# Optimization experiments

Measured on AMD Instinct MI355X. Metric: run time of the kernel, lower is better.

Reference implementation:

```python
import jax, jax.numpy as jnp
import numpy as np

N_NODES = 50000
N_EDGES = 600000
CH = 128


def _mlp(h, w1, b1, w2, b2):
    # Linear -> ReLU -> Linear (weights stored [in, out])
    return jax.nn.relu(h @ w1 + b1) @ w2 + b2


def setup_inputs() -> dict:
    key = jax.random.key(0)
    ks = jax.random.split(key, 12)
    def lin(k, fan_in, fan_out):
        bound = 1.0 / np.sqrt(fan_in)
        kw, kb = jax.random.split(k)
        w = jax.random.uniform(kw, (fan_in, fan_out), jnp.float32, -bound, bound)
        b = jax.random.uniform(kb, (fan_out,), jnp.float32, -bound, bound)
        return w, b
    ew1, eb1 = lin(ks[0], 3 * CH, CH)
    ew2, eb2 = lin(ks[1], CH, CH)
    nw1, nb1 = lin(ks[2], 2 * CH, CH)
    nw2, nb2 = lin(ks[3], CH, CH)
    x = jax.random.normal(ks[4], (N_NODES, CH), jnp.float32)
    edge_attr = jax.random.normal(ks[5], (N_EDGES, CH), jnp.float32)
    edge_index = jax.random.randint(ks[6], (2, N_EDGES), 0, N_NODES, jnp.int64 if jax.config.read('jax_enable_x64') else jnp.int32)
    return {"x": x, "edge_index": edge_index, "edge_attr": edge_attr,
            "ew1": ew1, "eb1": eb1, "ew2": ew2, "eb2": eb2,
            "nw1": nw1, "nb1": nb1, "nw2": nw2, "nb2": nb2}


def reference(x, edge_index, edge_attr, ew1, eb1, ew2, eb2, nw1, nb1, nw2, nb2):
    row, col = edge_index[0], edge_index[1]
    n = x.shape[0]
    # edge model: concat(source, target, edge_attr) -> MLP -> new edge_attr
    e_in = jnp.concatenate([x[row], x[col], edge_attr], axis=1)  # [E, 3*ch]
    new_edge_attr = _mlp(e_in, ew1, eb1, ew2, eb2)               # [E, ch]
    # node model: concat(x[col], new_edge_attr) -> MLP -> scatter_mean over row
    n_in = jnp.concatenate([x[col], new_edge_attr], axis=1)      # [E, 2*ch]
    msg = _mlp(n_in, nw1, nb1, nw2, nb2)                         # [E, ch]
    seg_sum = jax.ops.segment_sum(msg, row, num_segments=n)      # [N, ch]
    cnt = jax.ops.segment_sum(jnp.ones((msg.shape[0],), msg.dtype), row, num_segments=n)
    new_x = seg_sum / jnp.maximum(cnt, 1.0)[:, None]             # scatter_mean
    return new_x, new_edge_attr
```

## Files before the change

### kernel.cpp

```cpp
#include <hip/hip_runtime.h>
#include <stdint.h>

#define NN 50000
#define NE 600000
#define CH 128
#define RT 2
#define EPB 128

typedef __attribute__((ext_vector_type(8))) short short8;
typedef __attribute__((ext_vector_type(4))) float f32x4;
typedef __attribute__((ext_vector_type(4))) uint32_t u32x4;

__device__ __forceinline__ ushort f2bf(float f) {
  union { float f; uint32_t u; } v; v.f = f;
  uint32_t u = v.u;
  return (ushort)((u + 0x7FFFu + ((u >> 16) & 1u)) >> 16);
}
__device__ __forceinline__ float bf2f(uint32_t u16) {
  union { uint32_t u; float f; } t; t.u = u16 << 16; return t.f;
}
__device__ __forceinline__ uint32_t cvtpk_bf16(float a, float b) {
  uint32_t r;
  asm("v_cvt_pk_bf16_f32 %0, %1, %2" : "=v"(r) : "v"(a), "v"(b));
  return r;
}

__global__ void prep_frag_k(const float* __restrict__ ew1, const float* __restrict__ ew2,
                            const float* __restrict__ nw1, const float* __restrict__ nw2,
                            ushort* __restrict__ wB) {
  int idx = blockIdx.x * 256 + threadIdx.x;
  if (idx >= 114688) return;
  const float* src; int local;
  if (idx < 49152)      { src = ew1; local = idx; }
  else if (idx < 65536) { src = ew2; local = idx - 49152; }
  else if (idx < 98304) { src = nw1; local = idx - 65536; }
  else                  { src = nw2; local = idx - 98304; }
  int ks   = local >> 12;
  int rem  = local & 4095;
  int nt   = rem >> 9;
  int t    = rem & 511;
  int lane = t >> 3, i = t & 7;
  int k = ks * 32 + (lane >> 4) * 8 + i;
  int n = nt * 16 + (lane & 15);
  wB[idx] = f2bf(src[k * 128 + n]);
}

__global__ void convert_x_k(const float* __restrict__ x, ushort* __restrict__ xb) {
  int i = blockIdx.x * 256 + threadIdx.x;
  if (i >= NN * CH / 4) return;
  const float4 f = reinterpret_cast<const float4*>(x)[i];
  ushort4 r;
  r.x = f2bf(f.x); r.y = f2bf(f.y); r.z = f2bf(f.z); r.w = f2bf(f.w);
  reinterpret_cast<ushort4*>(xb)[i] = r;
}

__global__ void rank_k(const int* __restrict__ ei, unsigned* __restrict__ cnt,
                       unsigned* __restrict__ rank) {
  int e = blockIdx.x * 256 + threadIdx.x;
  if (e < NE) rank[e] = atomicAdd(&cnt[ei[e]], 1u);
}

__global__ void scan_k(const unsigned* __restrict__ cnt, unsigned* __restrict__ start) {
  __shared__ unsigned s[1024];
  const int CHUNK = (NN + 1023) / 1024;
  int t = threadIdx.x;
  int lo = t * CHUNK, hi = lo + CHUNK < NN ? lo + CHUNK : NN;
  unsigned sum = 0;
  for (int i = lo; i < hi; ++i) sum += cnt[i];
  s[t] = sum;
  __syncthreads();
  for (int off = 1; off < 1024; off <<= 1) {
    unsigned v = (t >= off) ? s[t - off] : 0u;
    __syncthreads();
    s[t] += v;
    __syncthreads();
  }
  unsigned run = t ? s[t - 1] : 0u;
  for (int i = lo; i < hi; ++i) { start[i] = run; run += cnt[i]; }
}

__global__ void dest_k(const int* __restrict__ ei, const unsigned* __restrict__ start,
                       const unsigned* __restrict__ rank, unsigned* __restrict__ dest) {
  int e = blockIdx.x * 256 + threadIdx.x;
  if (e < NE) dest[e] = start[ei[e]] + rank[e];
}

__device__ __forceinline__ void mm8(const ushort* Bcbuf, int lane,
                                    const short8 a[RT], f32x4 acc[RT][8]) {
#pragma unroll
  for (int nt = 0; nt < 8; ++nt) {
    short8 b = *reinterpret_cast<const short8*>(Bcbuf + nt * 512 + lane * 8);
#pragma unroll
    for (int rt = 0; rt < RT; ++rt)
      acc[rt][nt] = __builtin_amdgcn_mfma_f32_16x16x32_bf16(a[rt], b, acc[rt][nt], 0, 0, 0);
  }
}

__global__ __launch_bounds__(256, 2) void fused_k(
    const int* __restrict__ ei, const float* __restrict__ edge_attr,
    const ushort* __restrict__ wB,
    const float* __restrict__ eb1, const float* __restrict__ eb2,
    const float* __restrict__ nb1, const float* __restrict__ nb2,
    const ushort* __restrict__ xb, const unsigned* __restrict__ dest,
    ushort* __restrict__ msg, float* __restrict__ out_e)
{
  __shared__ ushort hbuf[4][RT * 16][136];
  __shared__ ushort Bc[4][4096];
  const int tid  = threadIdx.x;
  const int lane = tid & 63;
  const int widx = tid >> 6;
  const int wbase = blockIdx.x * EPB + widx * (RT * 16);
  const int l15 = lane & 15;
  const int g = lane >> 4;
  const int kg = g * 8;
  ushort (*h)[136] = hbuf[widx];

  short8 bt[2][4];

#define LDB2(set, ph) do { \
    const ushort* _s = wB + (size_t)(ph) * 4096 + tid * 16; \
    bt[set][0] = *reinterpret_cast<const short8*>(_s); \
    bt[set][1] = *reinterpret_cast<const short8*>(_s + 8); \
    bt[set][2] = *reinterpret_cast<const short8*>(_s + 4096); \
    bt[set][3] = *reinterpret_cast<const short8*>(_s + 4096 + 8); \
  } while (0)
#define STB2(set, ph) do { \
    ushort* _d0 = &Bc[(ph) & 3][tid * 16]; \
    ushort* _d1 = &Bc[((ph) + 1) & 3][tid * 16]; \
    *reinterpret_cast<short8*>(_d0)     = bt[set][0]; \
    *reinterpret_cast<short8*>(_d0 + 8) = bt[set][1]; \
    *reinterpret_cast<short8*>(_d1)     = bt[set][2]; \
    *reinterpret_cast<short8*>(_d1 + 8) = bt[set][3]; \
  } while (0)
#define STEP(s, A0, A1, DO_LDB, DO_STB) do { \
    __syncthreads(); \
    __builtin_amdgcn_s_setprio(1); \
    mm8(Bc[(2 * (s)) & 3], lane, A0, acc); \
    mm8(Bc[(2 * (s) + 1) & 3], lane, A1, acc); \
    __builtin_amdgcn_s_setprio(0); \
    if (DO_LDB) LDB2((s) & 1, 2 * (s) + 4); \
    if (DO_STB) STB2(((s) + 1) & 1, 2 * (s) + 2); \
  } while (0)
#define LDH(dst, ksl) do { \
    _Pragma("unroll") \
    for (int _rt = 0; _rt < RT; ++_rt) \
      dst[_rt] = *reinterpret_cast<const short8*>(&h[_rt * 16 + l15][(ksl) * 32 + kg]); \
  } while (0)

  LDB2(0, 0);
  LDB2(1, 2);

  int rowA[RT], colA[RT], eAc[RT];
#pragma unroll
  for (int rt = 0; rt < RT; ++rt) {
    int e = wbase + rt * 16 + l15;
    eAc[rt] = e < NE ? e : NE - 1;
    rowA[rt] = ei[eAc[rt]];
    colA[rt] = ei[NE + eAc[rt]];
  }
  short8 axr[4][RT], axc[4][RT];
#pragma unroll
  for (int ksl = 0; ksl < 4; ++ksl)
#pragma unroll
    for (int rt = 0; rt < RT; ++rt) {
      axr[ksl][rt] = *reinterpret_cast<const short8*>(xb + rowA[rt] * CH + ksl * 32 + kg);
      axc[ksl][rt] = *reinterpret_cast<const short8*>(xb + colA[rt] * CH + ksl * 32 + kg);
    }
  short8 eab[4][RT];
#pragma unroll
  for (int ksl = 0; ksl < 4; ++ksl)
#pragma unroll
    for (int rt = 0; rt < RT; ++rt) {
      const float* pp = edge_attr + (size_t)eAc[rt] * CH + ksl * 32 + kg;
      float4 f0 = *reinterpret_cast<const float4*>(pp);
      float4 f1 = *reinterpret_cast<const float4*>(pp + 4);
      union { u32x4 u; short8 s; } cv;
      cv.u = (u32x4){ cvtpk_bf16(f0.x, f0.y), cvtpk_bf16(f0.z, f0.w),
                      cvtpk_bf16(f1.x, f1.y), cvtpk_bf16(f1.z, f1.w) };
      eab[ksl][rt] = cv.s;
    }
  unsigned dp[RT * 4];
#pragma unroll
  for (int it = 0; it < RT * 4; ++it) {
    int er = wbase + it * 4 + g;
    dp[it] = dest[er < NE ? er : NE - 1];
  }

  STB2(0, 0);

  const f32x4 zero4 = {0.f, 0.f, 0.f, 0.f};
  f32x4 acc[RT][8];
  short8 ha0[RT], ha1[RT];

#pragma unroll
  for (int rt = 0; rt < RT; ++rt)
#pragma unroll
    for (int nt = 0; nt < 8; ++nt) acc[rt][nt] = zero4;

  STEP(0, axr[0], axr[1], 1, 1);
  STEP(1, axr[2], axr[3], 1, 1);
  STEP(2, axc[0], axc[1], 1, 1);
  STEP(3, axc[2], axc[3], 1, 1);
  STEP(4, eab[0], eab[1], 1, 1);
  STEP(5, eab[2], eab[3], 1, 1);
#pragma unroll
  for (int nt = 0; nt < 8; ++nt) {
    float bb = eb1[nt * 16 + l15];
#pragma unroll
    for (int rt = 0; rt < RT; ++rt)
#pragma unroll
      for (int r = 0; r < 4; r += 2) {
        float v0 = fmaxf(acc[rt][nt][r] + bb, 0.f);
        float v1 = fmaxf(acc[rt][nt][r + 1] + bb, 0.f);
        uint32_t pk = cvtpk_bf16(v0, v1);
        h[rt * 16 + g * 4 + r][nt * 16 + l15]     = (ushort)(pk & 0xffffu);
        h[rt * 16 + g * 4 + r + 1][nt * 16 + l15] = (ushort)(pk >> 16);
      }
  }

#pragma unroll
  for (int rt = 0; rt < RT; ++rt)
#pragma unroll
    for (int nt = 0; nt < 8; ++nt) acc[rt][nt] = zero4;
  LDH(ha0, 0); LDH(ha1, 1);
  STEP(6, ha0, ha1, 1, 1);
  LDH(ha0, 2); LDH(ha1, 3);
  STEP(7, ha0, ha1, 1, 1);
#pragma unroll
  for (int nt = 0; nt < 8; ++nt) {
    float bb = eb2[nt * 16 + l15];
#pragma unroll
    for (int rt = 0; rt < RT; ++rt) {
      float v[4];
#pragma unroll
      for (int r = 0; r < 4; ++r) {
        v[r] = acc[rt][nt][r] + bb;
        int erow = wbase + rt * 16 + g * 4 + r;
        if (erow < NE) out_e[(size_t)erow * CH + nt * 16 + l15] = v[r];
      }
#pragma unroll
      for (int r = 0; r < 4; r += 2) {
        uint32_t pk = cvtpk_bf16(v[r], v[r + 1]);
        h[rt * 16 + g * 4 + r][nt * 16 + l15]     = (ushort)(pk & 0xffffu);
        h[rt * 16 + g * 4 + r + 1][nt * 16 + l15] = (ushort)(pk >> 16);
      }
    }
  }

#pragma unroll
  for (int rt = 0; rt < RT; ++rt)
#pragma unroll
    for (int nt = 0; nt < 8; ++nt) acc[rt][nt] = zero4;
  STEP(8, axc[0], axc[1], 1, 1);
  STEP(9, axc[2], axc[3], 1, 1);
  LDH(ha0, 0); LDH(ha1, 1);
  STEP(10, ha0, ha1, 1, 1);
  LDH(ha0, 2); LDH(ha1, 3);
  STEP(11, ha0, ha1, 1, 1);
#pragma unroll
  for (int nt = 0; nt < 8; ++nt) {
    float bb = nb1[nt * 16 + l15];
#pragma unroll
    for (int rt = 0; rt < RT; ++rt)
#pragma unroll
      for (int r = 0; r < 4; r += 2) {
        float v0 = fmaxf(acc[rt][nt][r] + bb, 0.f);
        float v1 = fmaxf(acc[rt][nt][r + 1] + bb, 0.f);
        uint32_t pk = cvtpk_bf16(v0, v1);
        h[rt * 16 + g * 4 + r][nt * 16 + l15]     = (ushort)(pk & 0xffffu);
        h[rt * 16 + g * 4 + r + 1][nt * 16 + l15] = (ushort)(pk >> 16);
      }
  }

#pragma unroll
  for (int rt = 0; rt < RT; ++rt)
#pragma unroll
    for (int nt = 0; nt < 8; ++nt) acc[rt][nt] = zero4;
  LDH(ha0, 0); LDH(ha1, 1);
  STEP(12, ha0, ha1, 0, 1);
  LDH(ha0, 2); LDH(ha1, 3);
  STEP(13, ha0, ha1, 0, 0);
#pragma unroll
  for (int nt = 0; nt < 8; ++nt) {
    float bb = nb2[nt * 16 + l15];
#pragma unroll
    for (int rt = 0; rt < RT; ++rt)
#pragma unroll
      for (int r = 0; r < 4; r += 2) {
        uint32_t pk = cvtpk_bf16(acc[rt][nt][r] + bb, acc[rt][nt][r + 1] + bb);
        h[rt * 16 + g * 4 + r][nt * 16 + l15]     = (ushort)(pk & 0xffffu);
        h[rt * 16 + g * 4 + r + 1][nt * 16 + l15] = (ushort)(pk >> 16);
      }
  }
#pragma unroll
  for (int it = 0; it < RT * 4; ++it) {
    int row = it * 4 + g;
    int er = wbase + row;
    int col = l15 * 8;
    short8 v = *reinterpret_cast<const short8*>(&h[row][col]);
    if (er < NE)
      *reinterpret_cast<short8*>(msg + (size_t)dp[it] * CH + col) = v;
  }
#undef LDB2
#undef STB2
#undef STEP
#undef LDH
}

__global__ __launch_bounds__(256) void reduce_k(const ushort* __restrict__ msg,
    const unsigned* __restrict__ cnt, const unsigned* __restrict__ start,
    float* __restrict__ out_x) {
  int w = blockIdx.x * 4 + (threadIdx.x >> 6);
  if (w >= NN) return;
  int lane = threadIdx.x & 63;
  unsigned deg = cnt[w], s = start[w];
  float a0 = 0.f, a1 = 0.f;
#pragma unroll 4
  for (unsigned j = 0; j < deg; ++j) {
    uint32_t pk = *reinterpret_cast<const uint32_t*>(msg + (size_t)(s + j) * CH + lane * 2);
    a0 += bf2f(pk & 0xffffu);
    a1 += bf2f(pk >> 16);
  }
  float inv = 1.0f / fmaxf((float)deg, 1.0f);
  float2 o; o.x = a0 * inv; o.y = a1 * inv;
  *reinterpret_cast<float2*>(out_x + (size_t)w * CH + lane * 2) = o;
}

extern "C" void kernel_launch(void* const* d_in, const int* in_sizes, int n_in,
                              void* d_out, int out_size, void* d_ws, size_t ws_size,
                              hipStream_t stream) {
  const float* x   = (const float*)d_in[0];
  const int*   ei  = (const int*)d_in[1];
  const float* ea  = (const float*)d_in[2];
  const float* ew1 = (const float*)d_in[3];
  const float* eb1 = (const float*)d_in[4];
  const float* ew2 = (const float*)d_in[5];
  const float* eb2 = (const float*)d_in[6];
  const float* nw1 = (const float*)d_in[7];
  const float* nb1 = (const float*)d_in[8];
  const float* nw2 = (const float*)d_in[9];
  const float* nb2 = (const float*)d_in[10];

  float* out_x = (float*)d_out;
  float* out_e = (float*)d_out + (size_t)NN * CH;

  char* wsb = (char*)d_ws;
  ushort*   msg    = (ushort*)wsb;
  ushort*   wB     = (ushort*)(wsb + 153600000);
  ushort*   xb     = (ushort*)(wsb + 153829376);
  unsigned* cnt    = (unsigned*)(wsb + 166629376);
  unsigned* start  = (unsigned*)(wsb + 166829376);
  unsigned* rank   = (unsigned*)(wsb + 167029376);
  unsigned* dest   = (unsigned*)(wsb + 169429376);

  hipMemsetAsync(cnt, 0, (size_t)NN * sizeof(unsigned), stream);

  prep_frag_k<<<448, 256, 0, stream>>>(ew1, ew2, nw1, nw2, wB);
  convert_x_k<<<(NN * CH / 4 + 255) / 256, 256, 0, stream>>>(x, xb);
  rank_k<<<(NE + 255) / 256, 256, 0, stream>>>(ei, cnt, rank);
  scan_k<<<1, 1024, 0, stream>>>(cnt, start);
  dest_k<<<(NE + 255) / 256, 256, 0, stream>>>(ei, start, rank, dest);

  int nblk = (NE + EPB - 1) / EPB;
  fused_k<<<nblk, 256, 0, stream>>>(ei, ea, wB, eb1, eb2, nb1, nb2, xb, dest, msg, out_e);

  reduce_k<<<(NN + 3) / 4, 256, 0, stream>>>(msg, cnt, start, out_x);
}
```

Measured before the change: 431.8 us.

## Use 8-wave blocks sharing weight staging and stage edge output through LDS

Doubles the fused kernel's block to 512 threads (8 waves, 256 edges per block), so each thread loads half as many weight fragments into the shared LDS buffer. Weight staging cost per edge drops and register use per thread falls. The edge-output store now goes through a per-wave LDS scratch so each row is written with float4 coalesced stores instead of scattered scalar stores. The extra LDS and larger blocks may change occupancy, and the unsynchronized per-wave scratch reuse relies on wave-level ordering.

```diff
diff --git a/kernel.cpp b/kernel.cpp
--- a/kernel.cpp
+++ b/kernel.cpp
@@ -5,7 +5,8 @@
 #define NE 600000
 #define CH 128
 #define RT 2
-#define EPB 128
+#define WAVES 8
+#define EPB (WAVES * 32)
 
 typedef __attribute__((ext_vector_type(8))) short short8;
 typedef __attribute__((ext_vector_type(4))) float f32x4;
@@ -96,7 +97,7 @@
   }
 }
 
-__global__ __launch_bounds__(256, 2) void fused_k(
+__global__ __launch_bounds__(512, 1) void fused_k(
     const int* __restrict__ ei, const float* __restrict__ edge_attr,
     const ushort* __restrict__ wB,
     const float* __restrict__ eb1, const float* __restrict__ eb2,
@@ -104,8 +105,9 @@
     const ushort* __restrict__ xb, const unsigned* __restrict__ dest,
     ushort* __restrict__ msg, float* __restrict__ out_e)
 {
-  __shared__ ushort hbuf[4][RT * 16][136];
+  __shared__ ushort hbuf[WAVES][RT * 16][136];
   __shared__ ushort Bc[4][4096];
+  __shared__ float  st32[WAVES][4][132];
   const int tid  = threadIdx.x;
   const int lane = tid & 63;
   const int widx = tid >> 6;
@@ -115,22 +117,15 @@
   const int kg = g * 8;
   ushort (*h)[136] = hbuf[widx];
 
-  short8 bt[2][4];
+  short8 bt[2][2];
 
 #define LDB2(set, ph) do { \
-    const ushort* _s = wB + (size_t)(ph) * 4096 + tid * 16; \
-    bt[set][0] = *reinterpret_cast<const short8*>(_s); \
-    bt[set][1] = *reinterpret_cast<const short8*>(_s + 8); \
-    bt[set][2] = *reinterpret_cast<const short8*>(_s + 4096); \
-    bt[set][3] = *reinterpret_cast<const short8*>(_s + 4096 + 8); \
+    bt[set][0] = *reinterpret_cast<const short8*>(wB + (size_t)(ph) * 4096 + tid * 8); \
+    bt[set][1] = *reinterpret_cast<const short8*>(wB + (size_t)((ph) + 1) * 4096 + tid * 8); \
   } while (0)
 #define STB2(set, ph) do { \
-    ushort* _d0 = &Bc[(ph) & 3][tid * 16]; \
-    ushort* _d1 = &Bc[((ph) + 1) & 3][tid * 16]; \
-    *reinterpret_cast<short8*>(_d0)     = bt[set][0]; \
-    *reinterpret_cast<short8*>(_d0 + 8) = bt[set][1]; \
-    *reinterpret_cast<short8*>(_d1)     = bt[set][2]; \
-    *reinterpret_cast<short8*>(_d1 + 8) = bt[set][3]; \
+    *reinterpret_cast<short8*>(&Bc[(ph) & 3][tid * 8])       = bt[set][0]; \
+    *reinterpret_cast<short8*>(&Bc[((ph) + 1) & 3][tid * 8]) = bt[set][1]; \
   } while (0)
 #define STEP(s, A0, A1, DO_LDB, DO_STB) do { \
     __syncthreads(); \
@@ -226,24 +221,34 @@
   STEP(6, ha0, ha1, 1, 1);
   LDH(ha0, 2); LDH(ha1, 3);
   STEP(7, ha0, ha1, 1, 1);
-#pragma unroll
-  for (int nt = 0; nt < 8; ++nt) {
-    float bb = eb2[nt * 16 + l15];
+  {
+    float bb2[8];
+#pragma unroll
+    for (int nt = 0; nt < 8; ++nt) bb2[nt] = eb2[nt * 16 + l15];
 #pragma unroll
     for (int rt = 0; rt < RT; ++rt) {
-      float v[4];
 #pragma unroll
       for (int r = 0; r < 4; ++r) {
-        v[r] = acc[rt][nt][r] + bb;
-        int erow = wbase + rt * 16 + g * 4 + r;
-        if (erow < NE) out_e[(size_t)erow * CH + nt * 16 + l15] = v[r];
+#pragma unroll
+        for (int nt = 0; nt < 8; ++nt)
+          st32[widx][g][nt * 16 + l15] = acc[rt][nt][r] + bb2[nt];
+        int row_l = lane >> 4;
+        int erow = wbase + rt * 16 + row_l * 4 + r;
+        float4 v0 = *reinterpret_cast<const float4*>(&st32[widx][row_l][l15 * 4]);
+        float4 v1 = *reinterpret_cast<const float4*>(&st32[widx][row_l][l15 * 4 + 64]);
+        if (erow < NE) {
+          *reinterpret_cast<float4*>(out_e + (size_t)erow * CH + l15 * 4)      = v0;
+          *reinterpret_cast<float4*>(out_e + (size_t)erow * CH + 64 + l15 * 4) = v1;
+        }
       }
 #pragma unroll
-      for (int r = 0; r < 4; r += 2) {
-        uint32_t pk = cvtpk_bf16(v[r], v[r + 1]);
-        h[rt * 16 + g * 4 + r][nt * 16 + l15]     = (ushort)(pk & 0xffffu);
-        h[rt * 16 + g * 4 + r + 1][nt * 16 + l15] = (ushort)(pk >> 16);
-      }
+      for (int nt = 0; nt < 8; ++nt)
+#pragma unroll
+        for (int r = 0; r < 4; r += 2) {
+          uint32_t pk = cvtpk_bf16(acc[rt][nt][r] + bb2[nt], acc[rt][nt][r + 1] + bb2[nt]);
+          h[rt * 16 + g * 4 + r][nt * 16 + l15]     = (ushort)(pk & 0xffffu);
+          h[rt * 16 + g * 4 + r + 1][nt * 16 + l15] = (ushort)(pk >> 16);
+        }
     }
   }
 
@@ -362,7 +367,7 @@
   dest_k<<<(NE + 255) / 256, 256, 0, stream>>>(ei, start, rank, dest);
 
   int nblk = (NE + EPB - 1) / EPB;
-  fused_k<<<nblk, 256, 0, stream>>>(ei, ea, wB, eb1, eb2, nb1, nb2, xb, dest, msg, out_e);
+  fused_k<<<nblk, 512, 0, stream>>>(ei, ea, wB, eb1, eb2, nb1, nb2, xb, dest, msg, out_e);
 
   reduce_k<<<(NN + 3) / 4, 256, 0, stream>>>(msg, cnt, start, out_x);
 }
```

After: 451.0 us. 1.04x slower.
